# Kernel optimization log

Hardware: AMD Instinct MI355X
Metric: run time of the kernel (lower is better)

## Reference

```python
import jax, jax.numpy as jnp
import numpy as np
from jax import lax

REP_THR = 0.6
BORDER = 10


def setup_inputs() -> dict:
    key = jax.random.key(0)
    # repeatability heatmap in [0, 1), NCHW
    repeatability = jax.random.uniform(key, (16, 1, 1536, 1536), dtype=jnp.float32)
    return {"repeatability": repeatability}


def _local_max(x):
    # 3x3 stride-1 max pool with padding=1 (torch pads with -inf for maxpool)
    return lax.reduce_window(
        x, -jnp.inf, lax.max,
        window_dimensions=(1, 1, 3, 3),
        window_strides=(1, 1, 1, 1),
        padding=((0, 0), (0, 0), (1, 1), (1, 1)),
    )


def reference(repeatability):
    B, C, H, W = repeatability.shape
    maxima = (repeatability == _local_max(repeatability)) & (repeatability >= REP_THR)
    # border mask: zero out a 10-pixel frame
    border = jnp.zeros((H, W), dtype=bool).at[BORDER:-BORDER, BORDER:-BORDER].set(True)
    maxima = maxima & border  # broadcasts over (B, C)
    # nonzero().t()[2:4] -> row/col (y, x) coordinates of surviving maxima, shape [2, K]
    idx = jnp.nonzero(maxima)  # tuple (b, c, y, x); dynamic-shaped, eager only
    return jnp.stack(idx)[2:4]
```

## Files before the change

kernel.cpp:

```cpp
#include <hip/hip_runtime.h>

#define W 1536
#define H 1536
#define NB 16
#define N (NB * H * W)
#define T_PX 16
#define BLOCK 256
#define PX_PER_BLOCK (BLOCK * T_PX)
#define NBLK (N / PX_PER_BLOCK)
#define REP_THR 0.6f

__global__ __launch_bounds__(BLOCK) void nms_pass1(const float* __restrict__ in,
                                                   unsigned short* __restrict__ masks,
                                                   unsigned int* __restrict__ counts) {
    const unsigned t = threadIdx.x;
    const unsigned gid = blockIdx.x * BLOCK + t;
    const unsigned s = gid * T_PX;
    const unsigned row = s / W;
    const unsigned yy = row % H;
    const unsigned x0 = s - row * W;
    unsigned bits = 0u;
    if (yy >= 10u && yy < (unsigned)(H - 10)) {
        const float* p = in + s;
        float r0[24], r1[24], r2[24];
#pragma unroll
        for (int k = 0; k < 6; ++k) {
            *(float4*)(r0 + 4 * k) = *(const float4*)(p - W - 4 + 4 * k);
            *(float4*)(r1 + 4 * k) = *(const float4*)(p - 4 + 4 * k);
            *(float4*)(r2 + 4 * k) = *(const float4*)(p + W - 4 + 4 * k);
        }
#pragma unroll
        for (int j = 0; j < T_PX; ++j) {
            float v = r1[j + 4];
            float m = fmaxf(fmaxf(r0[j + 3], r0[j + 4]), r0[j + 5]);
            m = fmaxf(m, fmaxf(r1[j + 3], r1[j + 5]));
            float m2 = fmaxf(fmaxf(r2[j + 3], r2[j + 4]), r2[j + 5]);
            m = fmaxf(fmaxf(m, m2), REP_THR);
            bits |= (v >= m) ? (1u << j) : 0u;
        }
        unsigned vmask = 0xFFFFu;
        if (x0 == 0u) vmask = 0xFC00u;
        else if (x0 == (unsigned)(W - T_PX)) vmask = 0x003Fu;
        bits &= vmask;
    }
    masks[gid] = (unsigned short)bits;
    unsigned cnt = __popc(bits);
#pragma unroll
    for (int o = 32; o > 0; o >>= 1) cnt += __shfl_down(cnt, o, 64);
    __shared__ unsigned wsum[BLOCK / 64];
    if ((t & 63u) == 0u) wsum[t >> 6] = cnt;
    __syncthreads();
    if (t == 0) counts[blockIdx.x] = wsum[0] + wsum[1] + wsum[2] + wsum[3];
}

__global__ __launch_bounds__(1024) void nms_scan(const unsigned int* __restrict__ counts,
                                                 unsigned int* __restrict__ offsets) {
    const int t = threadIdx.x;
    const int lane = t & 63, wv = t >> 6;
    unsigned v[9];
    unsigned sum = 0;
#pragma unroll
    for (int k = 0; k < 9; ++k) { v[k] = counts[t * 9 + k]; sum += v[k]; }
    unsigned incl = sum;
#pragma unroll
    for (int o = 1; o < 64; o <<= 1) {
        unsigned u = __shfl_up(incl, o, 64);
        if (lane >= o) incl += u;
    }
    __shared__ unsigned wtot[16];
    if (lane == 63) wtot[wv] = incl;
    __syncthreads();
    unsigned wbase = 0;
#pragma unroll
    for (int k = 0; k < 16; ++k) wbase += (k < wv) ? wtot[k] : 0u;
    unsigned base = wbase + incl - sum;
#pragma unroll
    for (int k = 0; k < 9; ++k) { offsets[t * 9 + k] = base; base += v[k]; }
}

__global__ __launch_bounds__(BLOCK) void nms_pass3(const unsigned short* __restrict__ masks,
                                                   const unsigned int* __restrict__ offsets,
                                                   int* __restrict__ out, unsigned int K) {
    const unsigned t = threadIdx.x;
    const unsigned lane = t & 63u, wv = t >> 6;
    const unsigned gid = blockIdx.x * BLOCK + t;
    unsigned bits = masks[gid];
    const unsigned cnt = __popc(bits);
    unsigned incl = cnt;
#pragma unroll
    for (int o = 1; o < 64; o <<= 1) {
        unsigned u = __shfl_up(incl, o, 64);
        if (lane >= o) incl += u;
    }
    __shared__ unsigned wtot[BLOCK / 64];
    if (lane == 63u) wtot[wv] = incl;
    __syncthreads();
    unsigned wbase = 0;
#pragma unroll
    for (int k = 0; k < BLOCK / 64; ++k) wbase += (k < wv) ? wtot[k] : 0u;
    unsigned pos = offsets[blockIdx.x] + wbase + incl - cnt;
    if (bits) {
        const unsigned s = gid * T_PX;
        const unsigned row = s / W;
        const int yy = (int)(row % H);
        const int x0 = (int)(s - row * W);
        while (bits) {
            int j = __builtin_ctz(bits);
            bits &= bits - 1u;
            if (pos < K) {
                out[pos] = yy;
                out[K + pos] = x0 + j;
            }
            ++pos;
        }
    }
}

extern "C" void kernel_launch(void* const* d_in, const int* in_sizes, int n_in,
                              void* d_out, int out_size, void* d_ws, size_t ws_size,
                              hipStream_t stream) {
    const float* in = (const float*)d_in[0];
    int* out = (int*)d_out;
    unsigned short* masks = (unsigned short*)d_ws;
    unsigned int* counts = (unsigned int*)((char*)d_ws + (size_t)(N / T_PX) * 2);
    unsigned int* offsets = counts + NBLK;
    const unsigned int K = (unsigned int)(out_size / 2);

    nms_pass1<<<NBLK, BLOCK, 0, stream>>>(in, masks, counts);
    nms_scan<<<1, 1024, 0, stream>>>(counts, offsets);
    nms_pass3<<<NBLK, BLOCK, 0, stream>>>(masks, offsets, out, K);
}
```

Measured before the change: 259.8 us.

## Fuse NMS mask, scan and compaction into one decoupled-lookback kernel

Replaces the three-kernel pipeline (mask+count, single-block scan, compaction) with one kernel that computes maxima bits per 64-pixel chunk, then uses a decoupled look-back prefix scan over per-block descriptors to get global output offsets and write coordinates directly. This removes the masks workspace round trip and two kernel launches, and reuses vertical max columns across a sliding window. In exchange it adds a memset, a serial inter-block dependency chain with spin-waiting, and it assumes blocks make forward progress in launch order.

```diff
diff --git a/kernel.cpp b/kernel.cpp
--- a/kernel.cpp
+++ b/kernel.cpp
@@ -3,114 +3,137 @@
 #define W 1536
 #define H 1536
 #define NB 16
-#define N (NB * H * W)
-#define T_PX 16
-#define BLOCK 256
-#define PX_PER_BLOCK (BLOCK * T_PX)
-#define NBLK (N / PX_PER_BLOCK)
+#define ROWS_PER_TILE 16
+#define CHUNKS_PER_ROW 24
+#define BLOCK (ROWS_PER_TILE * CHUNKS_PER_ROW)
+#define NBLK (NB * H / ROWS_PER_TILE)
 #define REP_THR 0.6f
 
-__global__ __launch_bounds__(BLOCK) void nms_pass1(const float* __restrict__ in,
-                                                   unsigned short* __restrict__ masks,
-                                                   unsigned int* __restrict__ counts) {
-    const unsigned t = threadIdx.x;
-    const unsigned gid = blockIdx.x * BLOCK + t;
-    const unsigned s = gid * T_PX;
-    const unsigned row = s / W;
-    const unsigned yy = row % H;
-    const unsigned x0 = s - row * W;
-    unsigned bits = 0u;
-    if (yy >= 10u && yy < (unsigned)(H - 10)) {
-        const float* p = in + s;
-        float r0[24], r1[24], r2[24];
-#pragma unroll
-        for (int k = 0; k < 6; ++k) {
-            *(float4*)(r0 + 4 * k) = *(const float4*)(p - W - 4 + 4 * k);
-            *(float4*)(r1 + 4 * k) = *(const float4*)(p - 4 + 4 * k);
-            *(float4*)(r2 + 4 * k) = *(const float4*)(p + W - 4 + 4 * k);
-        }
-#pragma unroll
-        for (int j = 0; j < T_PX; ++j) {
-            float v = r1[j + 4];
-            float m = fmaxf(fmaxf(r0[j + 3], r0[j + 4]), r0[j + 5]);
-            m = fmaxf(m, fmaxf(r1[j + 3], r1[j + 5]));
-            float m2 = fmaxf(fmaxf(r2[j + 3], r2[j + 4]), r2[j + 5]);
-            m = fmaxf(fmaxf(m, m2), REP_THR);
-            bits |= (v >= m) ? (1u << j) : 0u;
-        }
-        unsigned vmask = 0xFFFFu;
-        if (x0 == 0u) vmask = 0xFC00u;
-        else if (x0 == (unsigned)(W - T_PX)) vmask = 0x003Fu;
-        bits &= vmask;
-    }
-    masks[gid] = (unsigned short)bits;
-    unsigned cnt = __popc(bits);
-#pragma unroll
-    for (int o = 32; o > 0; o >>= 1) cnt += __shfl_down(cnt, o, 64);
-    __shared__ unsigned wsum[BLOCK / 64];
-    if ((t & 63u) == 0u) wsum[t >> 6] = cnt;
-    __syncthreads();
-    if (t == 0) counts[blockIdx.x] = wsum[0] + wsum[1] + wsum[2] + wsum[3];
+__device__ __forceinline__ float max3f(float a, float b, float c) {
+    return fmaxf(fmaxf(a, b), c);
 }
 
-__global__ __launch_bounds__(1024) void nms_scan(const unsigned int* __restrict__ counts,
-                                                 unsigned int* __restrict__ offsets) {
-    const int t = threadIdx.x;
-    const int lane = t & 63, wv = t >> 6;
-    unsigned v[9];
-    unsigned sum = 0;
-#pragma unroll
-    for (int k = 0; k < 9; ++k) { v[k] = counts[t * 9 + k]; sum += v[k]; }
-    unsigned incl = sum;
-#pragma unroll
-    for (int o = 1; o < 64; o <<= 1) {
-        unsigned u = __shfl_up(incl, o, 64);
-        if (lane >= o) incl += u;
-    }
-    __shared__ unsigned wtot[16];
-    if (lane == 63) wtot[wv] = incl;
-    __syncthreads();
-    unsigned wbase = 0;
-#pragma unroll
-    for (int k = 0; k < 16; ++k) wbase += (k < wv) ? wtot[k] : 0u;
-    unsigned base = wbase + incl - sum;
-#pragma unroll
-    for (int k = 0; k < 9; ++k) { offsets[t * 9 + k] = base; base += v[k]; }
-}
-
-__global__ __launch_bounds__(BLOCK) void nms_pass3(const unsigned short* __restrict__ masks,
-                                                   const unsigned int* __restrict__ offsets,
+__global__ __launch_bounds__(BLOCK) void nms_fused(const float* __restrict__ in,
+                                                   unsigned long long* __restrict__ desc,
                                                    int* __restrict__ out, unsigned int K) {
     const unsigned t = threadIdx.x;
-    const unsigned lane = t & 63u, wv = t >> 6;
-    const unsigned gid = blockIdx.x * BLOCK + t;
-    unsigned bits = masks[gid];
-    const unsigned cnt = __popc(bits);
+    const unsigned lane = t & 63u;
+    const unsigned wv = t >> 6;
+    const unsigned blk = blockIdx.x;
+    const unsigned b = blk / 96u;
+    const unsigned ytile = blk - b * 96u;
+    const unsigned r = t / CHUNKS_PER_ROW;
+    const unsigned c = t - r * CHUNKS_PER_ROW;
+    const unsigned yy = ytile * ROWS_PER_TILE + r;
+
+    unsigned long long bits = 0ull;
+    if (yy >= 10u && yy < (unsigned)(H - 10)) {
+        const float* base = in + ((size_t)(b * H + yy) - 1) * W + c * 64u;
+        float4 a0 = *(const float4*)(base);
+        float4 a1 = *(const float4*)(base + W);
+        float4 a2 = *(const float4*)(base + 2 * W);
+        float4 p0 = *(const float4*)(base - 4);
+        float4 p1 = *(const float4*)(base + W - 4);
+        float4 p2 = *(const float4*)(base + 2 * W - 4);
+        float pw = max3f(p0.w, p1.w, p2.w);
+        float4 vc;
+        vc.x = max3f(a0.x, a1.x, a2.x);
+        vc.y = max3f(a0.y, a1.y, a2.y);
+        vc.z = max3f(a0.z, a1.z, a2.z);
+        vc.w = max3f(a0.w, a1.w, a2.w);
+        float4 ctr = a1;
+#pragma unroll 4
+        for (int k = 0; k < 16; ++k) {
+            float4 n0 = *(const float4*)(base + (4 * k + 4));
+            float4 n1 = *(const float4*)(base + W + (4 * k + 4));
+            float4 n2 = *(const float4*)(base + 2 * W + (4 * k + 4));
+            float4 vn;
+            vn.x = max3f(n0.x, n1.x, n2.x);
+            vn.y = max3f(n0.y, n1.y, n2.y);
+            vn.z = max3f(n0.z, n1.z, n2.z);
+            vn.w = max3f(n0.w, n1.w, n2.w);
+            unsigned g = 0;
+            g |= (ctr.x >= fmaxf(max3f(pw,   vc.x, vc.y), REP_THR)) ? 1u : 0u;
+            g |= (ctr.y >= fmaxf(max3f(vc.x, vc.y, vc.z), REP_THR)) ? 2u : 0u;
+            g |= (ctr.z >= fmaxf(max3f(vc.y, vc.z, vc.w), REP_THR)) ? 4u : 0u;
+            g |= (ctr.w >= fmaxf(max3f(vc.z, vc.w, vn.x), REP_THR)) ? 8u : 0u;
+            bits |= (unsigned long long)g << (4 * k);
+            pw = vc.w; vc = vn; ctr = n1;
+        }
+        if (c == 0u) bits &= ~0x3FFull;
+        if (c == (unsigned)(CHUNKS_PER_ROW - 1)) bits &= (1ull << 54) - 1ull;
+    }
+
+    unsigned cnt = (unsigned)__popcll(bits);
     unsigned incl = cnt;
 #pragma unroll
     for (int o = 1; o < 64; o <<= 1) {
         unsigned u = __shfl_up(incl, o, 64);
-        if (lane >= o) incl += u;
+        if (lane >= (unsigned)o) incl += u;
     }
     __shared__ unsigned wtot[BLOCK / 64];
+    __shared__ unsigned sPrefix;
     if (lane == 63u) wtot[wv] = incl;
     __syncthreads();
-    unsigned wbase = 0;
+    unsigned wbase = 0, total = 0;
 #pragma unroll
-    for (int k = 0; k < BLOCK / 64; ++k) wbase += (k < wv) ? wtot[k] : 0u;
-    unsigned pos = offsets[blockIdx.x] + wbase + incl - cnt;
+    for (int k = 0; k < BLOCK / 64; ++k) {
+        unsigned wtk = wtot[k];
+        wbase += ((unsigned)k < wv) ? wtk : 0u;
+        total += wtk;
+    }
+
+    if (t == 0u && blk != 0u)
+        __hip_atomic_store(&desc[blk], ((unsigned long long)total << 2) | 1ull,
+                           __ATOMIC_RELEASE, __HIP_MEMORY_SCOPE_AGENT);
+    if (wv == 0u) {
+        unsigned prefix = 0u;
+        if (blk != 0u) {
+            int wend = (int)blk;
+            for (;;) {
+                int idx = wend - 64 + (int)lane;
+                unsigned long long d;
+                for (;;) {
+                    d = (idx >= 0)
+                        ? __hip_atomic_load(&desc[idx], __ATOMIC_ACQUIRE, __HIP_MEMORY_SCOPE_AGENT)
+                        : 2ull;
+                    if (__all((d & 3ull) != 0ull)) break;
+                    __builtin_amdgcn_s_sleep(1);
+                }
+                unsigned long long pm = __ballot((d & 3ull) == 2ull);
+                unsigned v = (unsigned)(d >> 2);
+                unsigned contrib;
+                if (pm) {
+                    unsigned hp = 63u - (unsigned)__builtin_clzll(pm);
+                    contrib = (lane >= hp) ? v : 0u;
+                } else {
+                    contrib = v;
+                }
+#pragma unroll
+                for (int o = 1; o < 64; o <<= 1) contrib += __shfl_xor(contrib, o, 64);
+                prefix += contrib;
+                if (pm) break;
+                wend -= 64;
+                if (wend <= 0) break;
+            }
+        }
+        if (lane == 0u) {
+            __hip_atomic_store(&desc[blk], ((unsigned long long)(prefix + total) << 2) | 2ull,
+                               __ATOMIC_RELEASE, __HIP_MEMORY_SCOPE_AGENT);
+            sPrefix = prefix;
+        }
+    }
+    __syncthreads();
+
+    unsigned pos = sPrefix + wbase + (incl - cnt);
     if (bits) {
-        const unsigned s = gid * T_PX;
-        const unsigned row = s / W;
-        const int yy = (int)(row % H);
-        const int x0 = (int)(s - row * W);
-        while (bits) {
-            int j = __builtin_ctz(bits);
-            bits &= bits - 1u;
-            if (pos < K) {
-                out[pos] = yy;
-                out[K + pos] = x0 + j;
-            }
+        const int x0 = (int)(c * 64u);
+        const int yv = (int)yy;
+        unsigned long long m = bits;
+        while (m) {
+            int j = __builtin_ctzll(m);
+            m &= m - 1ull;
+            if (pos < K) { out[pos] = yv; out[K + pos] = x0 + j; }
             ++pos;
         }
     }
@@ -121,12 +144,8 @@
                               hipStream_t stream) {
     const float* in = (const float*)d_in[0];
     int* out = (int*)d_out;
-    unsigned short* masks = (unsigned short*)d_ws;
-    unsigned int* counts = (unsigned int*)((char*)d_ws + (size_t)(N / T_PX) * 2);
-    unsigned int* offsets = counts + NBLK;
-    const unsigned int K = (unsigned int)(out_size / 2);
-
-    nms_pass1<<<NBLK, BLOCK, 0, stream>>>(in, masks, counts);
-    nms_scan<<<1, 1024, 0, stream>>>(counts, offsets);
-    nms_pass3<<<NBLK, BLOCK, 0, stream>>>(masks, offsets, out, K);
+    unsigned long long* desc = (unsigned long long*)d_ws;
+    const unsigned K = (unsigned)(out_size / 2);
+    hipMemsetAsync(d_ws, 0, NBLK * sizeof(unsigned long long), stream);
+    nms_fused<<<NBLK, BLOCK, 0, stream>>>(in, desc, out, K);
 }
```

After: 904.9 us. 3.48x slower.
